# Optimization experiments

Hardware: AMD Instinct MI355X
Metric: run time of the kernel (lower is better)

## Reference

```python
import jax, jax.numpy as jnp
import numpy as np

N_NODES = 100000
D_FEAT = 128
N_EDGES = 500000


def setup_inputs() -> dict:
    key = jax.random.key(0)
    k1, k2, k3 = jax.random.split(key, 3)
    h = jax.random.normal(k1, (N_NODES, D_FEAT), dtype=jnp.float32)
    src = jax.random.randint(k2, (N_EDGES,), 0, N_NODES, dtype=jnp.int64)
    dst = jax.random.randint(k3, (N_EDGES,), 0, N_NODES, dtype=jnp.int64)
    return {"h": h, "src": src, "dst": dst}


def reference(h, src, dst):
    # DGL fn.u_dot_v('h','h','score'): per-edge dot of source and dest
    # node features; result shape [E, 1] (dot keeps a trailing dim of 1).
    u = h[src]  # [E, D]
    v = h[dst]  # [E, D]
    score = jnp.sum(u * v, axis=-1, keepdims=True)  # [E, 1]
    return score
```

## Files before the change

kernel.cpp:

```cpp
#include <hip/hip_runtime.h>
#include <stdint.h>


__global__ __launch_bounds__(256) void quant_i8_kernel(
    const float* __restrict__ h,
    uint32_t* __restrict__ q,
    float* __restrict__ scales,
    int n_rows)
{
    const int gid = blockIdx.x * blockDim.x + threadIdx.x;
    const int row = gid >> 5;
    const int sl  = gid & 31;
    if (row >= n_rows) return;

    const float4 f = *reinterpret_cast<const float4*>(h + (size_t)row * 128 + sl * 4);

    float m = fmaxf(fmaxf(fabsf(f.x), fabsf(f.y)), fmaxf(fabsf(f.z), fabsf(f.w)));
    #pragma unroll
    for (int off = 16; off > 0; off >>= 1)
        m = fmaxf(m, __shfl_xor(m, off, 32));

    const float inv = (m > 0.f) ? 127.0f / m : 0.f;

    int i0 = (int)rintf(fminf(fmaxf(f.x * inv, -127.f), 127.f));
    int i1 = (int)rintf(fminf(fmaxf(f.y * inv, -127.f), 127.f));
    int i2 = (int)rintf(fminf(fmaxf(f.z * inv, -127.f), 127.f));
    int i3 = (int)rintf(fminf(fmaxf(f.w * inv, -127.f), 127.f));

    const uint32_t packed = (uint32_t)(i0 & 0xFF)        |
                            ((uint32_t)(i1 & 0xFF) << 8)  |
                            ((uint32_t)(i2 & 0xFF) << 16) |
                            ((uint32_t)(i3 & 0xFF) << 24);
    q[(size_t)row * 32 + sl] = packed;

    if (sl == 0)
        scales[row] = m * (1.0f / 127.0f);
}

__device__ __forceinline__ int dot4_i8(uint32_t a, uint32_t b, int acc) {
#if defined(__has_builtin) && __has_builtin(__builtin_amdgcn_sdot4)
    return __builtin_amdgcn_sdot4((int)a, (int)b, acc, false);
#else
    #pragma unroll
    for (int k = 0; k < 4; ++k) {
        const int av = (int)(int8_t)((a >> (8 * k)) & 0xFF);
        const int bv = (int)(int8_t)((b >> (8 * k)) & 0xFF);
        acc += av * bv;
    }
    return acc;
#endif
}

constexpr int EPG = 4;

__global__ __launch_bounds__(256) void edge_dot_i8_kernel(
    const uint32_t* __restrict__ q,
    const float* __restrict__ scales,
    const int* __restrict__ src,
    const int* __restrict__ dst,
    float* __restrict__ out,
    int n_edges)
{
    const int gid   = blockIdx.x * blockDim.x + threadIdx.x;
    const int group = gid >> 3;
    const int lane  = gid & 7;
    const int ebase = group * EPG;
    if (ebase >= n_edges) return;

    if (ebase + EPG <= n_edges) {
        int s[EPG], d[EPG];
        #pragma unroll
        for (int i = 0; i < EPG; ++i) {
            s[i] = src[ebase + i];
            d[i] = dst[ebase + i];
        }

        float sa[EPG], sb[EPG];
        #pragma unroll
        for (int i = 0; i < EPG; ++i) {
            sa[i] = scales[s[i]];
            sb[i] = scales[d[i]];
        }

        uint4 a[EPG], b[EPG];
        #pragma unroll
        for (int i = 0; i < EPG; ++i) {
            a[i] = *reinterpret_cast<const uint4*>(q + (size_t)s[i] * 32 + lane * 4);
            b[i] = *reinterpret_cast<const uint4*>(q + (size_t)d[i] * 32 + lane * 4);
        }

        #pragma unroll
        for (int i = 0; i < EPG; ++i) {
            int acc = 0;
            acc = dot4_i8(a[i].x, b[i].x, acc);
            acc = dot4_i8(a[i].y, b[i].y, acc);
            acc = dot4_i8(a[i].z, b[i].z, acc);
            acc = dot4_i8(a[i].w, b[i].w, acc);
            #pragma unroll
            for (int off = 4; off > 0; off >>= 1)
                acc += __shfl_down(acc, off, 8);
            if (lane == 0)
                out[ebase + i] = (float)acc * sa[i] * sb[i];
        }
    } else {
        for (int e = ebase; e < n_edges; ++e) {
            const int s = src[e];
            const int d = dst[e];
            const float sc = scales[s] * scales[d];
            const uint4 av = *reinterpret_cast<const uint4*>(q + (size_t)s * 32 + lane * 4);
            const uint4 bv = *reinterpret_cast<const uint4*>(q + (size_t)d * 32 + lane * 4);
            int acc = 0;
            acc = dot4_i8(av.x, bv.x, acc);
            acc = dot4_i8(av.y, bv.y, acc);
            acc = dot4_i8(av.z, bv.z, acc);
            acc = dot4_i8(av.w, bv.w, acc);
            #pragma unroll
            for (int off = 4; off > 0; off >>= 1)
                acc += __shfl_down(acc, off, 8);
            if (lane == 0)
                out[e] = (float)acc * sc;
        }
    }
}

extern "C" void kernel_launch(void* const* d_in, const int* in_sizes, int n_in,
                              void* d_out, int out_size, void* d_ws, size_t ws_size,
                              hipStream_t stream)
{
    const float* h   = (const float*)d_in[0];
    const int*   src = (const int*)d_in[1];
    const int*   dst = (const int*)d_in[2];
    float*       out = (float*)d_out;

    const int n_feat_total = in_sizes[0];
    const int n_edges      = in_sizes[1];
    const int n_rows       = n_feat_total / 128;

    uint32_t* q      = (uint32_t*)d_ws;
    float*    scales = (float*)((char*)d_ws + (size_t)n_rows * 128);

    const int qblocks = (n_rows * 32 + 255) / 256;
    quant_i8_kernel<<<qblocks, 256, 0, stream>>>(h, q, scales, n_rows);

    const int groups = (n_edges + EPG - 1) / EPG;
    const int blocks = (groups * 8 + 255) / 256;
    edge_dot_i8_kernel<<<blocks, 256, 0, stream>>>(q, scales, src, dst, out, n_edges);
}
```

Baseline: 105.7 us.

## Split int8 feature rows into chunk-major slabs and reduce edge partials in separate pass

Stores the quantized features chunk-major as four 32-byte slabs per row. The edge kernel becomes one thread per edge per chunk, writing integer partial dot products to a workspace buffer, and a third combine kernel sums the partials and applies the scales. The aim is a smaller per-chunk working set that stays in cache during the random gathers. In exchange it adds a kernel launch, extra traffic for the partials, and rereads src/dst four times plus once more in the combine step.

```diff
diff --git a/kernel.cpp b/kernel.cpp
--- a/kernel.cpp
+++ b/kernel.cpp
@@ -1,6 +1,9 @@
 #include <hip/hip_runtime.h>
 #include <stdint.h>
 
+
+#define N_CHUNK 4
+#define CHUNK_UINTS 8
 
 __global__ __launch_bounds__(256) void quant_i8_kernel(
     const float* __restrict__ h,
@@ -31,7 +34,9 @@
                             ((uint32_t)(i1 & 0xFF) << 8)  |
                             ((uint32_t)(i2 & 0xFF) << 16) |
                             ((uint32_t)(i3 & 0xFF) << 24);
-    q[(size_t)row * 32 + sl] = packed;
+
+    const int chunk = sl >> 3;
+    q[((size_t)chunk * n_rows + row) * CHUNK_UINTS + (sl & 7)] = packed;
 
     if (sl == 0)
         scales[row] = m * (1.0f / 127.0f);
@@ -51,76 +56,59 @@
 #endif
 }
 
-constexpr int EPG = 4;
+__global__ __launch_bounds__(256) void edge_partial_kernel(
+    const uint32_t* __restrict__ q,
+    const int* __restrict__ src,
+    const int* __restrict__ dst,
+    int* __restrict__ partial,
+    int n_edges, int blocks_per_chunk, int n_rows)
+{
+    const int chunk = blockIdx.x / blocks_per_chunk;
+    const int e = (blockIdx.x - chunk * blocks_per_chunk) * blockDim.x + threadIdx.x;
+    if (e >= n_edges) return;
 
-__global__ __launch_bounds__(256) void edge_dot_i8_kernel(
-    const uint32_t* __restrict__ q,
+    const int s = __builtin_nontemporal_load(src + e);
+    const int d = __builtin_nontemporal_load(dst + e);
+
+    const uint32_t* qc = q + (size_t)chunk * n_rows * CHUNK_UINTS;
+    const uint4* pa = reinterpret_cast<const uint4*>(qc + (size_t)s * CHUNK_UINTS);
+    const uint4* pb = reinterpret_cast<const uint4*>(qc + (size_t)d * CHUNK_UINTS);
+
+    const uint4 a0 = pa[0];
+    const uint4 a1 = pa[1];
+    const uint4 b0 = pb[0];
+    const uint4 b1 = pb[1];
+
+    int acc = 0;
+    acc = dot4_i8(a0.x, b0.x, acc);
+    acc = dot4_i8(a0.y, b0.y, acc);
+    acc = dot4_i8(a0.z, b0.z, acc);
+    acc = dot4_i8(a0.w, b0.w, acc);
+    acc = dot4_i8(a1.x, b1.x, acc);
+    acc = dot4_i8(a1.y, b1.y, acc);
+    acc = dot4_i8(a1.z, b1.z, acc);
+    acc = dot4_i8(a1.w, b1.w, acc);
+
+    __builtin_nontemporal_store(acc, partial + (size_t)chunk * n_edges + e);
+}
+
+__global__ __launch_bounds__(256) void combine_kernel(
+    const int* __restrict__ partial,
     const float* __restrict__ scales,
     const int* __restrict__ src,
     const int* __restrict__ dst,
     float* __restrict__ out,
     int n_edges)
 {
-    const int gid   = blockIdx.x * blockDim.x + threadIdx.x;
-    const int group = gid >> 3;
-    const int lane  = gid & 7;
-    const int ebase = group * EPG;
-    if (ebase >= n_edges) return;
+    const int e = blockIdx.x * blockDim.x + threadIdx.x;
+    if (e >= n_edges) return;
 
-    if (ebase + EPG <= n_edges) {
-        int s[EPG], d[EPG];
-        #pragma unroll
-        for (int i = 0; i < EPG; ++i) {
-            s[i] = src[ebase + i];
-            d[i] = dst[ebase + i];
-        }
+    const int p = partial[e]
+                + partial[e + (size_t)n_edges]
+                + partial[e + (size_t)2 * n_edges]
+                + partial[e + (size_t)3 * n_edges];
 
-        float sa[EPG], sb[EPG];
-        #pragma unroll
-        for (int i = 0; i < EPG; ++i) {
-            sa[i] = scales[s[i]];
-            sb[i] = scales[d[i]];
-        }
-
-        uint4 a[EPG], b[EPG];
-        #pragma unroll
-        for (int i = 0; i < EPG; ++i) {
-            a[i] = *reinterpret_cast<const uint4*>(q + (size_t)s[i] * 32 + lane * 4);
-            b[i] = *reinterpret_cast<const uint4*>(q + (size_t)d[i] * 32 + lane * 4);
-        }
-
-        #pragma unroll
-        for (int i = 0; i < EPG; ++i) {
-            int acc = 0;
-            acc = dot4_i8(a[i].x, b[i].x, acc);
-            acc = dot4_i8(a[i].y, b[i].y, acc);
-            acc = dot4_i8(a[i].z, b[i].z, acc);
-            acc = dot4_i8(a[i].w, b[i].w, acc);
-            #pragma unroll
-            for (int off = 4; off > 0; off >>= 1)
-                acc += __shfl_down(acc, off, 8);
-            if (lane == 0)
-                out[ebase + i] = (float)acc * sa[i] * sb[i];
-        }
-    } else {
-        for (int e = ebase; e < n_edges; ++e) {
-            const int s = src[e];
-            const int d = dst[e];
-            const float sc = scales[s] * scales[d];
-            const uint4 av = *reinterpret_cast<const uint4*>(q + (size_t)s * 32 + lane * 4);
-            const uint4 bv = *reinterpret_cast<const uint4*>(q + (size_t)d * 32 + lane * 4);
-            int acc = 0;
-            acc = dot4_i8(av.x, bv.x, acc);
-            acc = dot4_i8(av.y, bv.y, acc);
-            acc = dot4_i8(av.z, bv.z, acc);
-            acc = dot4_i8(av.w, bv.w, acc);
-            #pragma unroll
-            for (int off = 4; off > 0; off >>= 1)
-                acc += __shfl_down(acc, off, 8);
-            if (lane == 0)
-                out[e] = (float)acc * sc;
-        }
-    }
+    out[e] = (float)p * scales[src[e]] * scales[dst[e]];
 }
 
 extern "C" void kernel_launch(void* const* d_in, const int* in_sizes, int n_in,
@@ -138,11 +126,14 @@
 
     uint32_t* q      = (uint32_t*)d_ws;
     float*    scales = (float*)((char*)d_ws + (size_t)n_rows * 128);
+    int*      partial = (int*)((char*)d_ws + (size_t)n_rows * 128 + (size_t)n_rows * 4);
 
     const int qblocks = (n_rows * 32 + 255) / 256;
     quant_i8_kernel<<<qblocks, 256, 0, stream>>>(h, q, scales, n_rows);
 
-    const int groups = (n_edges + EPG - 1) / EPG;
-    const int blocks = (groups * 8 + 255) / 256;
-    edge_dot_i8_kernel<<<blocks, 256, 0, stream>>>(q, scales, src, dst, out, n_edges);
+    const int bpc = (n_edges + 255) / 256;
+    edge_partial_kernel<<<bpc * N_CHUNK, 256, 0, stream>>>(
+        q, src, dst, partial, n_edges, bpc, n_rows);
+
+    combine_kernel<<<bpc, 256, 0, stream>>>(partial, scales, src, dst, out, n_edges);
 }
```

Result: slower. 131.6 us (+24.5%).
